# Optimization experiments

Hardware: AMD Instinct MI355X
Metric: run time of the kernel (lower is better)

## Reference

```python
import jax, jax.numpy as jnp
import numpy as np

H = 16      # num_heads
D = 64      # nhid (per-head dim)
SL, BS = 1024, 64
DM = 1024   # keys_dim == query_dim == values_dim

def setup_inputs() -> dict:
    key = jax.random.key(0)
    k1, k2, k3, k4, k5 = jax.random.split(key, 5)
    return {
        "query":  jax.random.normal(k1, (BS, DM), dtype=jnp.float32),
        "keys":   jax.random.normal(k2, (SL, BS, DM), dtype=jnp.float32),
        "values": jax.random.normal(k3, (SL, BS, DM), dtype=jnp.float32),
        "Wq":     jax.random.normal(k4, (H * D, DM), dtype=jnp.float32) * 0.02,
        "Wk":     jax.random.normal(k5, (H * D, DM), dtype=jnp.float32) * 0.02,
    }

def reference(query, keys, values, Wq, Wk):
    bs = query.shape[0]
    sl = keys.shape[0]
    scale = jnp.asarray(np.sqrt(D), dtype=query.dtype)
    # projections (note: original module applies keys_linear to values -- a bug we replicate)
    qp = (query @ Wq.T).reshape(bs, H, D)                 # [bs, H, D]
    kp = (keys @ Wk.T).reshape(sl, bs, H, D)              # [sl, bs, H, D]
    vp = (values @ Wk.T).reshape(sl, bs, H, D)            # [sl, bs, H, D]
    # per-head scaled dot-product scores, softmax over the sequence axis (dim 0)
    scores = jnp.einsum('bhd,sbhd->sbh', qp, kp) / scale  # [sl, bs, H]
    attn = jax.nn.softmax(scores, axis=0)
    out = jnp.einsum('sbh,sbhd->bhd', attn, vp)           # [bs, H, D]
    return out.reshape(bs, H * D)
```

## Files before the change

### kernel.cpp

```cpp
#include <hip/hip_runtime.h>
#include <cstddef>
#include <cstdint>

#define NH 16
#define HD 64
#define SLEN 1024
#define NB 64
#define DMODEL 1024

#define DOT4_ACC(acc, k, q) \
  acc = fmaf((k).x, (q).x, fmaf((k).y, (q).y, fmaf((k).z, (q).z, fmaf((k).w, (q).w, (acc)))))

#define FMA4_BCAST(accv, qv, w0_, w1_, w2_, w3_) do { \
  (accv).x = fmaf((qv).x, (w0_).x, fmaf((qv).y, (w1_).x, fmaf((qv).z, (w2_).x, fmaf((qv).w, (w3_).x, (accv).x)))); \
  (accv).y = fmaf((qv).x, (w0_).y, fmaf((qv).y, (w1_).y, fmaf((qv).z, (w2_).y, fmaf((qv).w, (w3_).y, (accv).y)))); \
  (accv).z = fmaf((qv).x, (w0_).z, fmaf((qv).y, (w1_).z, fmaf((qv).z, (w2_).z, fmaf((qv).w, (w3_).z, (accv).z)))); \
  (accv).w = fmaf((qv).x, (w0_).w, fmaf((qv).y, (w1_).w, fmaf((qv).z, (w2_).w, fmaf((qv).w, (w3_).w, (accv).w)))); \
} while (0)

#define VMCNT_WAIT(n) asm volatile("s_waitcnt vmcnt(" #n ")" ::: "memory")
#define BAR() asm volatile("s_barrier" ::: "memory")

__device__ __forceinline__ float wred_sum(float v) {
#pragma unroll
  for (int off = 32; off; off >>= 1) v += __shfl_xor(v, off, 64);
  return v;
}

__device__ __forceinline__ void gload16(const float* g, float* lds_base) {
  __builtin_amdgcn_global_load_lds(
      (const __attribute__((address_space(1))) void*)g,
      (__attribute__((address_space(3))) void*)lds_base, 16, 0, 0);
}

__global__ __launch_bounds__(256) void k0_qp(const float* __restrict__ query,
                                             const float* __restrict__ Wq,
                                             float* __restrict__ qp) {
  const int tid = threadIdx.x;
  const int w = tid >> 6, l = tid & 63;
  const int jq = blockIdx.x & 255;
  const int bq = blockIdx.x >> 8;
  const int j = jq * 4 + w;
  const float4* wr = reinterpret_cast<const float4*>(Wq + (size_t)j * DMODEL) + l * 4;
  const float4 w0 = wr[0], w1 = wr[1], w2 = wr[2], w3 = wr[3];
  float acc[16];
#pragma unroll
  for (int bi = 0; bi < 16; ++bi) {
    const float4* qr = reinterpret_cast<const float4*>(
        query + (size_t)(bq * 16 + bi) * DMODEL) + l * 4;
    float4 q0 = qr[0], q1 = qr[1], q2 = qr[2], q3 = qr[3];
    float s = 0.f;
    DOT4_ACC(s, w0, q0); DOT4_ACC(s, w1, q1); DOT4_ACC(s, w2, q2); DOT4_ACC(s, w3, q3);
    acc[bi] = s;
  }
#pragma unroll
  for (int off = 32; off; off >>= 1) {
#pragma unroll
    for (int bi = 0; bi < 16; ++bi) acc[bi] += __shfl_xor(acc[bi], off, 64);
  }
  if (l == 0) {
#pragma unroll
    for (int bi = 0; bi < 16; ++bi)
      qp[(size_t)(bq * 16 + bi) * DMODEL + j] = acc[bi];
  }
}

__global__ __launch_bounds__(256) void k1_qt(const float* __restrict__ qp,
                                             const float* __restrict__ Wk,
                                             float* __restrict__ qt) {
  __shared__ __align__(16) float qpl[2][HD];
  const int h = blockIdx.x & 15;
  const int b0 = (blockIdx.x >> 4) * 2;
  const int tid = threadIdx.x;
  if (tid < 2 * HD) qpl[tid >> 6][tid & 63] =
      qp[(size_t)(b0 + (tid >> 6)) * DMODEL + h * HD + (tid & 63)];
  __syncthreads();
  const int m4 = tid * 4;
  float4 acc0 = make_float4(0.f, 0.f, 0.f, 0.f);
  float4 acc1 = make_float4(0.f, 0.f, 0.f, 0.f);
  const float* wbase = Wk + (size_t)(h * HD) * DMODEL + m4;
  for (int d = 0; d < HD; d += 4) {
    float4 wk0 = *reinterpret_cast<const float4*>(wbase + (size_t)(d + 0) * DMODEL);
    float4 wk1 = *reinterpret_cast<const float4*>(wbase + (size_t)(d + 1) * DMODEL);
    float4 wk2 = *reinterpret_cast<const float4*>(wbase + (size_t)(d + 2) * DMODEL);
    float4 wk3 = *reinterpret_cast<const float4*>(wbase + (size_t)(d + 3) * DMODEL);
    float4 qa = *reinterpret_cast<const float4*>(&qpl[0][d]);
    float4 qb = *reinterpret_cast<const float4*>(&qpl[1][d]);
    FMA4_BCAST(acc0, qa, wk0, wk1, wk2, wk3);
    FMA4_BCAST(acc1, qb, wk0, wk1, wk2, wk3);
  }
  *reinterpret_cast<float4*>(qt + ((size_t)(b0 + 0) * NH + h) * DMODEL + m4) = acc0;
  *reinterpret_cast<float4*>(qt + ((size_t)(b0 + 1) * NH + h) * DMODEL + m4) = acc1;
}

__global__ __launch_bounds__(256, 2) void k2_scores(const float* __restrict__ keys,
                                                    const float* __restrict__ qt,
                                                    float* __restrict__ scp) {
  __shared__ __align__(16) float kb[2][256 * 32];
  __shared__ __align__(16) float qb[2][NH * 32];
  const int b  = blockIdx.x & 63;
  const int st = (blockIdx.x >> 6) & 3;
  const int mh = blockIdx.x >> 8;
  const int tid = threadIdx.x, w = tid >> 6, l = tid & 63;
  const int ms = l & 3;
  const int rg = (l >> 2) & 7;
  const int hq = l >> 5;
  const int s0 = st * 256;
  const size_t rowstride = (size_t)NB * DMODEL;
  const float* kbase = keys + ((size_t)s0 * NB + b) * DMODEL + mh * 512;
  const float* qbase = qt + (size_t)b * NH * DMODEL + mh * 512;
  const int srow  = l >> 3;
  const int sslot = l & 7;

#define K2_STAGE(buf_, ch_) do {                                               \
    _Pragma("unroll")                                                          \
    for (int i_ = 0; i_ < 8; ++i_) {                                           \
      const int r_ = w * 64 + i_ * 8 + srow;                                   \
      gload16(kbase + (size_t)r_ * rowstride + (ch_) * 32 +                    \
                  ((sslot ^ srow) << 2),                                       \
              &kb[buf_][(w * 64 + i_ * 8) * 32]);                              \
    }                                                                          \
    if (w < 2)                                                                 \
      gload16(qbase + (size_t)(w * 8 + srow) * DMODEL + (ch_) * 32 +           \
                  ((sslot ^ srow) << 2),                                       \
              &qb[buf_][w * 8 * 32]);                                          \
  } while (0)

  float acc[8][8];
#pragma unroll
  for (int r = 0; r < 8; ++r)
#pragma unroll
    for (int h = 0; h < 8; ++h) acc[r][h] = 0.f;

  K2_STAGE(0, 0);
  for (int ch = 0; ch < 16; ++ch) {
    const int buf = ch & 1;
    if (ch + 1 < 16) {
      K2_STAGE(buf ^ 1, ch + 1);
      if (w < 2) { VMCNT_WAIT(9); } else { VMCNT_WAIT(8); }
    } else {
      VMCNT_WAIT(0);
    }
    BAR();
#pragma unroll
    for (int j = 0; j < 2; ++j) {
      const int c = j * 4 + ms;
      float4 kv[8], qv[8];
#pragma unroll
      for (int r = 0; r < 8; ++r) {
        const int row = w * 64 + rg * 8 + r;
        kv[r] = *reinterpret_cast<const float4*>(
            &kb[buf][row * 32 + ((c ^ r) << 2)]);
      }
#pragma unroll
      for (int h = 0; h < 8; ++h) {
        const int hh = hq * 8 + h;
        qv[h] = *reinterpret_cast<const float4*>(
            &qb[buf][hh * 32 + ((c ^ h) << 2)]);
      }
#pragma unroll
      for (int r = 0; r < 8; ++r)
#pragma unroll
        for (int h = 0; h < 8; ++h)
          DOT4_ACC(acc[r][h], kv[r], qv[h]);
    }
    BAR();
  }
#undef K2_STAGE
#pragma unroll
  for (int r = 0; r < 8; ++r)
#pragma unroll
    for (int h = 0; h < 8; ++h) {
      acc[r][h] += __shfl_xor(acc[r][h], 1, 64);
      acc[r][h] += __shfl_xor(acc[r][h], 2, 64);
    }
  const float scale = 0.125f;
  float* plane = scp + (size_t)mh * NB * NH * SLEN;
#pragma unroll
  for (int r = 0; r < 8; ++r) {
#pragma unroll
    for (int t = 0; t < 2; ++t) {
      float v = ms == 0 ? acc[r][t] : ms == 1 ? acc[r][2 + t]
              : ms == 2 ? acc[r][4 + t] : acc[r][6 + t];
      plane[((size_t)b * NH + hq * 8 + ms * 2 + t) * SLEN
            + s0 + w * 64 + rg * 8 + r] = v * scale;
    }
  }
}

__global__ __launch_bounds__(256) void k_sm(float* __restrict__ sc0,
                                            const float* __restrict__ sc1) {
  __shared__ float red[8];
  const int tid = threadIdx.x, w = tid >> 6, l = tid & 63;
  float* p0 = sc0 + (size_t)blockIdx.x * SLEN;
  const float* p1 = sc1 + (size_t)blockIdx.x * SLEN;
  float4 xa = reinterpret_cast<const float4*>(p0)[tid];
  float4 xb = reinterpret_cast<const float4*>(p1)[tid];
  float4 x = make_float4(xa.x + xb.x, xa.y + xb.y, xa.z + xb.z, xa.w + xb.w);
  float mx = fmaxf(fmaxf(x.x, x.y), fmaxf(x.z, x.w));
#pragma unroll
  for (int off = 32; off; off >>= 1) mx = fmaxf(mx, __shfl_xor(mx, off, 64));
  if (l == 0) red[w] = mx;
  __syncthreads();
  mx = fmaxf(fmaxf(red[0], red[1]), fmaxf(red[2], red[3]));
  float4 e;
  e.x = __expf(x.x - mx); e.y = __expf(x.y - mx);
  e.z = __expf(x.z - mx); e.w = __expf(x.w - mx);
  float sum = e.x + e.y + e.z + e.w;
  sum = wred_sum(sum);
  if (l == 0) red[4 + w] = sum;
  __syncthreads();
  sum = red[4] + red[5] + red[6] + red[7];
  const float inv = 1.f / sum;
  e.x *= inv; e.y *= inv; e.z *= inv; e.w *= inv;
  reinterpret_cast<float4*>(p0)[tid] = e;
}

template <int NCH>
__global__ __launch_bounds__(256) void k3_cpart(const float* __restrict__ values,
                                                const float* __restrict__ attn,
                                                float* __restrict__ cp) {
  constexpr int SC = SLEN / NCH;
  __shared__ __align__(16) float vb[2][4][DMODEL];
  __shared__ __align__(16) float al[NH][SC];
  const int b = blockIdx.x & 63;
  const int ch = blockIdx.x >> 6;
  const int s0 = ch * SC;
  const int tid = threadIdx.x, w = tid >> 6, l = tid & 63;
  for (int f = tid; f < NH * (SC / 4); f += 256) {
    int hh = f / (SC / 4), c4 = (f % (SC / 4)) * 4;
    *reinterpret_cast<float4*>(&al[hh][c4]) = *reinterpret_cast<const float4*>(
        attn + ((size_t)b * NH + hh) * SLEN + s0 + c4);
  }
  const int m4 = tid * 4;
  float4 acc[NH];
#pragma unroll
  for (int i = 0; i < NH; ++i) acc[i] = make_float4(0.f, 0.f, 0.f, 0.f);
  const size_t rowstride = (size_t)NB * DMODEL;
  const float* vbase = values + ((size_t)s0 * NB + b) * DMODEL;

#define K3_STAGE(buf_, g_) do {                                               \
    const float* rg_ = vbase + (size_t)((g_) * 4 + w) * rowstride;            \
    _Pragma("unroll")                                                         \
    for (int j_ = 0; j_ < 4; ++j_)                                            \
      gload16(rg_ + j_ * 256 + l * 4, &vb[buf_][w][j_ * 256]);                \
  } while (0)

  K3_STAGE(0, 0);
  __syncthreads();
  for (int g = 0; g < SC / 4; ++g) {
    const int buf = g & 1;
    if (g + 1 < SC / 4) {
      K3_STAGE(buf ^ 1, g + 1);
      VMCNT_WAIT(4);
    } else {
      VMCNT_WAIT(0);
    }
    BAR();
    float4 v0 = *reinterpret_cast<const float4*>(&vb[buf][0][m4]);
    float4 v1 = *reinterpret_cast<const float4*>(&vb[buf][1][m4]);
    float4 v2 = *reinterpret_cast<const float4*>(&vb[buf][2][m4]);
    float4 v3 = *reinterpret_cast<const float4*>(&vb[buf][3][m4]);
#pragma unroll
    for (int hh = 0; hh < NH; ++hh) {
      float4 av = *reinterpret_cast<const float4*>(&al[hh][g * 4]);
      FMA4_BCAST(acc[hh], av, v0, v1, v2, v3);
    }
    BAR();
  }
#undef K3_STAGE
#pragma unroll
  for (int hh = 0; hh < NH; ++hh)
    *reinterpret_cast<float4*>(cp + (((size_t)ch * NB + b) * NH + hh) * DMODEL + m4) = acc[hh];
}

template <int NCH>
__global__ __launch_bounds__(256) void k4_out(const float* __restrict__ cp,
                                              const float* __restrict__ Wk,
                                              float* __restrict__ out) {
  __shared__ __align__(16) float cl[2 * DMODEL];
  const int h = blockIdx.x & 15;
  const int b0 = (blockIdx.x >> 4) * 2;
  const int tid = threadIdx.x, w = tid >> 6, l = tid & 63;
  for (int f = tid; f < 2 * DMODEL / 4; f += 256) {
    int bi = f >> 8, m4 = (f & 255) * 4;
    float4 s = make_float4(0.f, 0.f, 0.f, 0.f);
#pragma unroll
    for (int ch = 0; ch < NCH; ++ch) {
      float4 t = *reinterpret_cast<const float4*>(
          cp + (((size_t)ch * NB + b0 + bi) * NH + h) * DMODEL + m4);
      s.x += t.x; s.y += t.y; s.z += t.z; s.w += t.w;
    }
    *reinterpret_cast<float4*>(&cl[bi * DMODEL + m4]) = s;
  }
  __syncthreads();
  float4 c[2][4];
#pragma unroll
  for (int bi = 0; bi < 2; ++bi)
#pragma unroll
    for (int k = 0; k < 4; ++k)
      c[bi][k] = *reinterpret_cast<const float4*>(&cl[bi * DMODEL + l * 16 + k * 4]);
  for (int jj = 0; jj < 16; ++jj) {
    const int d = w * 16 + jj;
    const float4* wr = reinterpret_cast<const float4*>(Wk + (size_t)(h * HD + d) * DMODEL) + l * 4;
    const float4 w0 = wr[0], w1 = wr[1], w2 = wr[2], w3 = wr[3];
#pragma unroll
    for (int bi = 0; bi < 2; ++bi) {
      float s = 0.f;
      DOT4_ACC(s, w0, c[bi][0]); DOT4_ACC(s, w1, c[bi][1]);
      DOT4_ACC(s, w2, c[bi][2]); DOT4_ACC(s, w3, c[bi][3]);
      s = wred_sum(s);
      if (l == 0) out[(size_t)(b0 + bi) * (NH * HD) + h * HD + d] = s;
    }
  }
}

extern "C" void kernel_launch(void* const* d_in, const int* in_sizes, int n_in,
                              void* d_out, int out_size, void* d_ws, size_t ws_size,
                              hipStream_t stream) {
  const float* query  = (const float*)d_in[0];
  const float* keys   = (const float*)d_in[1];
  const float* values = (const float*)d_in[2];
  const float* Wq     = (const float*)d_in[3];
  const float* Wk     = (const float*)d_in[4];
  float* out = (float*)d_out;

  float* W   = (float*)d_ws;
  float* qp  = W;
  float* qt  = qp + (size_t)NB * DMODEL;
  float* sc0 = qt + (size_t)NB * NH * DMODEL;
  float* sc1 = sc0 + (size_t)NB * NH * SLEN;
  float* cp  = sc1 + (size_t)NB * NH * SLEN;

  const size_t base_floats = (size_t)NB * DMODEL + (size_t)NB * NH * DMODEL
                           + 2 * (size_t)NB * NH * SLEN;

  k0_qp<<<1024, 256, 0, stream>>>(query, Wq, qp);
  k1_qt<<<512, 256, 0, stream>>>(qp, Wk, qt);
  k2_scores<<<512, 256, 0, stream>>>(keys, qt, sc0);
  k_sm<<<NB * NH, 256, 0, stream>>>(sc0, sc1);

  const size_t chunk_floats = (size_t)NB * NH * DMODEL;
  if (ws_size >= (base_floats + 16 * chunk_floats) * sizeof(float)) {
    k3_cpart<16><<<16 * NB, 256, 0, stream>>>(values, sc0, cp);
    k4_out<16><<<NH * (NB / 2), 256, 0, stream>>>(cp, Wk, out);
  } else if (ws_size >= (base_floats + 8 * chunk_floats) * sizeof(float)) {
    k3_cpart<8><<<8 * NB, 256, 0, stream>>>(values, sc0, cp);
    k4_out<8><<<NH * (NB / 2), 256, 0, stream>>>(cp, Wk, out);
  } else {
    k3_cpart<4><<<4 * NB, 256, 0, stream>>>(values, sc0, cp);
    k4_out<4><<<NH * (NB / 2), 256, 0, stream>>>(cp, Wk, out);
  }
}
```

Baseline: 207.4 us.

## Split score kernel into single-wave blocks with wider chunks and no barriers

```diff
diff --git a/kernel.cpp b/kernel.cpp
--- a/kernel.cpp
+++ b/kernel.cpp
@@ -93,37 +93,41 @@
   *reinterpret_cast<float4*>(qt + ((size_t)(b0 + 1) * NH + h) * DMODEL + m4) = acc1;
 }
 
-__global__ __launch_bounds__(256, 2) void k2_scores(const float* __restrict__ keys,
-                                                    const float* __restrict__ qt,
-                                                    float* __restrict__ scp) {
-  __shared__ __align__(16) float kb[2][256 * 32];
-  __shared__ __align__(16) float qb[2][NH * 32];
+__global__ __launch_bounds__(64) void k2_scores(const float* __restrict__ keys,
+                                                const float* __restrict__ qt,
+                                                float* __restrict__ scp) {
+  __shared__ __align__(16) float kb[2][64 * 64];
+  __shared__ __align__(16) float qb[2][NH * 64];
   const int b  = blockIdx.x & 63;
-  const int st = (blockIdx.x >> 6) & 3;
-  const int mh = blockIdx.x >> 8;
-  const int tid = threadIdx.x, w = tid >> 6, l = tid & 63;
+  const int st = (blockIdx.x >> 6) & 15;
+  const int mh = blockIdx.x >> 10;
+  const int l = threadIdx.x;
   const int ms = l & 3;
   const int rg = (l >> 2) & 7;
   const int hq = l >> 5;
-  const int s0 = st * 256;
+  const int s0 = st * 64;
   const size_t rowstride = (size_t)NB * DMODEL;
   const float* kbase = keys + ((size_t)s0 * NB + b) * DMODEL + mh * 512;
   const float* qbase = qt + (size_t)b * NH * DMODEL + mh * 512;
-  const int srow  = l >> 3;
-  const int sslot = l & 7;
+  const int srow  = l >> 4;
+  const int sslot = l & 15;
 
 #define K2_STAGE(buf_, ch_) do {                                               \
     _Pragma("unroll")                                                          \
-    for (int i_ = 0; i_ < 8; ++i_) {                                           \
-      const int r_ = w * 64 + i_ * 8 + srow;                                   \
-      gload16(kbase + (size_t)r_ * rowstride + (ch_) * 32 +                    \
-                  ((sslot ^ srow) << 2),                                       \
-              &kb[buf_][(w * 64 + i_ * 8) * 32]);                              \
+    for (int i_ = 0; i_ < 16; ++i_) {                                          \
+      const int r_ = i_ * 4 + srow;                                            \
+      const int sw_ = ((r_ >> 3) ^ r_) & 15;                                   \
+      gload16(kbase + (size_t)r_ * rowstride + (ch_) * 64 +                    \
+                  ((sslot ^ sw_) << 2),                                        \
+              &kb[buf_][(i_ * 4) * 64]);                                       \
     }                                                                          \
-    if (w < 2)                                                                 \
-      gload16(qbase + (size_t)(w * 8 + srow) * DMODEL + (ch_) * 32 +           \
-                  ((sslot ^ srow) << 2),                                       \
-              &qb[buf_][w * 8 * 32]);                                          \
+    _Pragma("unroll")                                                          \
+    for (int i_ = 0; i_ < 4; ++i_) {                                           \
+      const int h_ = i_ * 4 + srow;                                            \
+      gload16(qbase + (size_t)h_ * DMODEL + (ch_) * 64 +                       \
+                  ((sslot ^ (h_ & 15)) << 2),                                  \
+              &qb[buf_][(i_ * 4) * 64]);                                       \
+    }                                                                          \
   } while (0)
 
   float acc[8][8];
@@ -133,30 +137,30 @@
     for (int h = 0; h < 8; ++h) acc[r][h] = 0.f;
 
   K2_STAGE(0, 0);
-  for (int ch = 0; ch < 16; ++ch) {
+  for (int ch = 0; ch < 8; ++ch) {
     const int buf = ch & 1;
-    if (ch + 1 < 16) {
+    if (ch + 1 < 8) {
       K2_STAGE(buf ^ 1, ch + 1);
-      if (w < 2) { VMCNT_WAIT(9); } else { VMCNT_WAIT(8); }
+      VMCNT_WAIT(20);
     } else {
       VMCNT_WAIT(0);
     }
-    BAR();
-#pragma unroll
-    for (int j = 0; j < 2; ++j) {
+#pragma unroll
+    for (int j = 0; j < 4; ++j) {
       const int c = j * 4 + ms;
       float4 kv[8], qv[8];
 #pragma unroll
       for (int r = 0; r < 8; ++r) {
-        const int row = w * 64 + rg * 8 + r;
+        const int row = rg * 8 + r;
+        const int sw = ((row >> 3) ^ row) & 15;
         kv[r] = *reinterpret_cast<const float4*>(
-            &kb[buf][row * 32 + ((c ^ r) << 2)]);
+            &kb[buf][row * 64 + ((c ^ sw) << 2)]);
       }
 #pragma unroll
       for (int h = 0; h < 8; ++h) {
         const int hh = hq * 8 + h;
         qv[h] = *reinterpret_cast<const float4*>(
-            &qb[buf][hh * 32 + ((c ^ h) << 2)]);
+            &qb[buf][hh * 64 + ((c ^ hh) << 2)]);
       }
 #pragma unroll
       for (int r = 0; r < 8; ++r)
@@ -164,7 +168,6 @@
         for (int h = 0; h < 8; ++h)
           DOT4_ACC(acc[r][h], kv[r], qv[h]);
     }
-    BAR();
   }
 #undef K2_STAGE
 #pragma unroll
@@ -183,7 +186,7 @@
       float v = ms == 0 ? acc[r][t] : ms == 1 ? acc[r][2 + t]
               : ms == 2 ? acc[r][4 + t] : acc[r][6 + t];
       plane[((size_t)b * NH + hq * 8 + ms * 2 + t) * SLEN
-            + s0 + w * 64 + rg * 8 + r] = v * scale;
+            + s0 + rg * 8 + r] = v * scale;
     }
   }
 }
@@ -337,7 +340,7 @@
 
   k0_qp<<<1024, 256, 0, stream>>>(query, Wq, qp);
   k1_qt<<<512, 256, 0, stream>>>(qp, Wk, qt);
-  k2_scores<<<512, 256, 0, stream>>>(keys, qt, sc0);
+  k2_scores<<<2048, 64, 0, stream>>>(keys, qt, sc0);
   k_sm<<<NB * NH, 256, 0, stream>>>(sc0, sc1);
 
   const size_t chunk_floats = (size_t)NB * NH * DMODEL;
```

Result: slower. 226.0 us (+9.0%).

## Retile score kernel over full model dim and drop split-plane partial sums

Applied to the files above, without the earlier changes.

```diff
diff --git a/kernel.cpp b/kernel.cpp
--- a/kernel.cpp
+++ b/kernel.cpp
@@ -93,37 +93,34 @@
   *reinterpret_cast<float4*>(qt + ((size_t)(b0 + 1) * NH + h) * DMODEL + m4) = acc1;
 }
 
-__global__ __launch_bounds__(256, 2) void k2_scores(const float* __restrict__ keys,
-                                                    const float* __restrict__ qt,
-                                                    float* __restrict__ scp) {
-  __shared__ __align__(16) float kb[2][256 * 32];
-  __shared__ __align__(16) float qb[2][NH * 32];
+__global__ __launch_bounds__(256) void k2_scores(const float* __restrict__ keys,
+                                                 const float* __restrict__ qt,
+                                                 float* __restrict__ sc) {
+  __shared__ __align__(16) float kb[2][32][256];
+  __shared__ __align__(16) float qb[2][NH][256];
   const int b  = blockIdx.x & 63;
-  const int st = (blockIdx.x >> 6) & 3;
-  const int mh = blockIdx.x >> 8;
+  const int st = blockIdx.x >> 6;
   const int tid = threadIdx.x, w = tid >> 6, l = tid & 63;
-  const int ms = l & 3;
-  const int rg = (l >> 2) & 7;
+  const int ms = l & 31;
   const int hq = l >> 5;
-  const int s0 = st * 256;
+  const int s0 = st * 32;
   const size_t rowstride = (size_t)NB * DMODEL;
-  const float* kbase = keys + ((size_t)s0 * NB + b) * DMODEL + mh * 512;
-  const float* qbase = qt + (size_t)b * NH * DMODEL + mh * 512;
-  const int srow  = l >> 3;
-  const int sslot = l & 7;
+  const float* kbase = keys + ((size_t)s0 * NB + b) * DMODEL;
+  const float* qbase = qt + (size_t)b * NH * DMODEL;
 
 #define K2_STAGE(buf_, ch_) do {                                               \
     _Pragma("unroll")                                                          \
     for (int i_ = 0; i_ < 8; ++i_) {                                           \
-      const int r_ = w * 64 + i_ * 8 + srow;                                   \
-      gload16(kbase + (size_t)r_ * rowstride + (ch_) * 32 +                    \
-                  ((sslot ^ srow) << 2),                                       \
-              &kb[buf_][(w * 64 + i_ * 8) * 32]);                              \
+      const int r_ = w * 8 + i_;                                               \
+      gload16(kbase + (size_t)(s0 * 0 + r_) * rowstride + (ch_) * 256 + l * 4, \
+              &kb[buf_][r_][0]);                                               \
     }                                                                          \
-    if (w < 2)                                                                 \
-      gload16(qbase + (size_t)(w * 8 + srow) * DMODEL + (ch_) * 32 +           \
-                  ((sslot ^ srow) << 2),                                       \
-              &qb[buf_][w * 8 * 32]);                                          \
+    _Pragma("unroll")                                                          \
+    for (int i_ = 0; i_ < 4; ++i_) {                                           \
+      const int h_ = w * 4 + i_;                                               \
+      gload16(qbase + (size_t)h_ * DMODEL + (ch_) * 256 + l * 4,               \
+              &qb[buf_][h_][0]);                                               \
+    }                                                                          \
   } while (0)
 
   float acc[8][8];
@@ -133,31 +130,27 @@
     for (int h = 0; h < 8; ++h) acc[r][h] = 0.f;
 
   K2_STAGE(0, 0);
-  for (int ch = 0; ch < 16; ++ch) {
+  VMCNT_WAIT(0);
+  __syncthreads();
+  for (int ch = 0; ch < 4; ++ch) {
     const int buf = ch & 1;
-    if (ch + 1 < 16) {
+    if (ch + 1 < 4) {
       K2_STAGE(buf ^ 1, ch + 1);
-      if (w < 2) { VMCNT_WAIT(9); } else { VMCNT_WAIT(8); }
+      VMCNT_WAIT(12);
     } else {
       VMCNT_WAIT(0);
     }
     BAR();
 #pragma unroll
     for (int j = 0; j < 2; ++j) {
-      const int c = j * 4 + ms;
+      const int c = j * 32 + ms;
       float4 kv[8], qv[8];
 #pragma unroll
-      for (int r = 0; r < 8; ++r) {
-        const int row = w * 64 + rg * 8 + r;
-        kv[r] = *reinterpret_cast<const float4*>(
-            &kb[buf][row * 32 + ((c ^ r) << 2)]);
-      }
-#pragma unroll
-      for (int h = 0; h < 8; ++h) {
-        const int hh = hq * 8 + h;
-        qv[h] = *reinterpret_cast<const float4*>(
-            &qb[buf][hh * 32 + ((c ^ h) << 2)]);
-      }
+      for (int r = 0; r < 8; ++r)
+        kv[r] = *reinterpret_cast<const float4*>(&kb[buf][w * 8 + r][c * 4]);
+#pragma unroll
+      for (int h = 0; h < 8; ++h)
+        qv[h] = *reinterpret_cast<const float4*>(&qb[buf][hq * 8 + h][c * 4]);
 #pragma unroll
       for (int r = 0; r < 8; ++r)
 #pragma unroll
@@ -168,35 +161,29 @@
   }
 #undef K2_STAGE
 #pragma unroll
-  for (int r = 0; r < 8; ++r)
-#pragma unroll
-    for (int h = 0; h < 8; ++h) {
-      acc[r][h] += __shfl_xor(acc[r][h], 1, 64);
-      acc[r][h] += __shfl_xor(acc[r][h], 2, 64);
-    }
+  for (int off = 1; off <= 16; off <<= 1)
+#pragma unroll
+    for (int r = 0; r < 8; ++r)
+#pragma unroll
+      for (int h = 0; h < 8; ++h)
+        acc[r][h] += __shfl_xor(acc[r][h], off, 64);
   const float scale = 0.125f;
-  float* plane = scp + (size_t)mh * NB * NH * SLEN;
-#pragma unroll
-  for (int r = 0; r < 8; ++r) {
+  {
+    const int r = ms >> 2;
+    const int hb = (ms & 3) * 2;
 #pragma unroll
     for (int t = 0; t < 2; ++t) {
-      float v = ms == 0 ? acc[r][t] : ms == 1 ? acc[r][2 + t]
-              : ms == 2 ? acc[r][4 + t] : acc[r][6 + t];
-      plane[((size_t)b * NH + hq * 8 + ms * 2 + t) * SLEN
-            + s0 + w * 64 + rg * 8 + r] = v * scale;
-    }
-  }
-}
-
-__global__ __launch_bounds__(256) void k_sm(float* __restrict__ sc0,
-                                            const float* __restrict__ sc1) {
+      const int h = hq * 8 + hb + t;
+      sc[((size_t)b * NH + h) * SLEN + s0 + w * 8 + r] = acc[r][hb + t] * scale;
+    }
+  }
+}
+
+__global__ __launch_bounds__(256) void k_sm(float* __restrict__ sc) {
   __shared__ float red[8];
   const int tid = threadIdx.x, w = tid >> 6, l = tid & 63;
-  float* p0 = sc0 + (size_t)blockIdx.x * SLEN;
-  const float* p1 = sc1 + (size_t)blockIdx.x * SLEN;
-  float4 xa = reinterpret_cast<const float4*>(p0)[tid];
-  float4 xb = reinterpret_cast<const float4*>(p1)[tid];
-  float4 x = make_float4(xa.x + xb.x, xa.y + xb.y, xa.z + xb.z, xa.w + xb.w);
+  float* p = sc + (size_t)blockIdx.x * SLEN;
+  float4 x = reinterpret_cast<const float4*>(p)[tid];
   float mx = fmaxf(fmaxf(x.x, x.y), fmaxf(x.z, x.w));
 #pragma unroll
   for (int off = 32; off; off >>= 1) mx = fmaxf(mx, __shfl_xor(mx, off, 64));
@@ -213,7 +200,7 @@
   sum = red[4] + red[5] + red[6] + red[7];
   const float inv = 1.f / sum;
   e.x *= inv; e.y *= inv; e.z *= inv; e.w *= inv;
-  reinterpret_cast<float4*>(p0)[tid] = e;
+  reinterpret_cast<float4*>(p)[tid] = e;
 }
 
 template <int NCH>
@@ -328,27 +315,26 @@
   float* W   = (float*)d_ws;
   float* qp  = W;
   float* qt  = qp + (size_t)NB * DMODEL;
-  float* sc0 = qt + (size_t)NB * NH * DMODEL;
-  float* sc1 = sc0 + (size_t)NB * NH * SLEN;
-  float* cp  = sc1 + (size_t)NB * NH * SLEN;
+  float* sc  = qt + (size_t)NB * NH * DMODEL;
+  float* cp  = sc + (size_t)NB * NH * SLEN;
 
   const size_t base_floats = (size_t)NB * DMODEL + (size_t)NB * NH * DMODEL
-                           + 2 * (size_t)NB * NH * SLEN;
+                           + (size_t)NB * NH * SLEN;
 
   k0_qp<<<1024, 256, 0, stream>>>(query, Wq, qp);
   k1_qt<<<512, 256, 0, stream>>>(qp, Wk, qt);
-  k2_scores<<<512, 256, 0, stream>>>(keys, qt, sc0);
-  k_sm<<<NB * NH, 256, 0, stream>>>(sc0, sc1);
+  k2_scores<<<2048, 256, 0, stream>>>(keys, qt, sc);
+  k_sm<<<NB * NH, 256, 0, stream>>>(sc);
 
   const size_t chunk_floats = (size_t)NB * NH * DMODEL;
   if (ws_size >= (base_floats + 16 * chunk_floats) * sizeof(float)) {
-    k3_cpart<16><<<16 * NB, 256, 0, stream>>>(values, sc0, cp);
+    k3_cpart<16><<<16 * NB, 256, 0, stream>>>(values, sc, cp);
     k4_out<16><<<NH * (NB / 2), 256, 0, stream>>>(cp, Wk, out);
   } else if (ws_size >= (base_floats + 8 * chunk_floats) * sizeof(float)) {
-    k3_cpart<8><<<8 * NB, 256, 0, stream>>>(values, sc0, cp);
+    k3_cpart<8><<<8 * NB, 256, 0, stream>>>(values, sc, cp);
     k4_out<8><<<NH * (NB / 2), 256, 0, stream>>>(cp, Wk, out);
   } else {
-    k3_cpart<4><<<4 * NB, 256, 0, stream>>>(values, sc0, cp);
+    k3_cpart<4><<<4 * NB, 256, 0, stream>>>(values, sc, cp);
     k4_out<4><<<NH * (NB / 2), 256, 0, stream>>>(cp, Wk, out);
   }
 }
```

Measured after the change: 270.1 us. 30.2% more time.
